# Kernel tuning notes

Measured on AMD Instinct MI355X. Metric: run time of the kernel, lower is better.

Reference implementation:

```python
import jax, jax.numpy as jnp
import numpy as np

B, DZ, DE, M, H = 4096, 2048, 128, 32, 1024
GATE_TEMP = 1.0


def setup_inputs() -> dict:
    key = jax.random.key(0)
    ks = jax.random.split(key, 6)
    s = lambda k, shape, sc: jax.random.normal(k, shape, dtype=jnp.float32) * sc
    return dict(
        z=s(ks[0], (B, DZ), 1.0),
        base_W=s(ks[1], (3, DZ), 0.02),
        base_b=jnp.zeros((3,), jnp.float32),
        gate_W=s(ks[2], (DE, DZ), 0.02),
        gate_b=jnp.zeros((DE,), jnp.float32),
        E=s(ks[3], (M, DE), 0.02),              # material embedding table
        W1=s(ks[4], (M, H, DZ + DE), 0.02),     # stacked first-layer weights
        b1=jnp.zeros((M, H), jnp.float32),
        W2=s(ks[5], (M, 3, H), 0.02),           # stacked second-layer weights
        b2=jnp.zeros((M, 3), jnp.float32),
    )


def _l2norm(x, eps=1e-12):
    # matches F.normalize(dim=-1): x / max(||x||_2, eps)
    n = jnp.linalg.norm(x, axis=-1, keepdims=True)
    return x / jnp.maximum(n, eps)


def reference(z, base_W, base_b, gate_W, gate_b, E, W1, b1, W2, b2):
    dz = z.shape[1]
    # base head: [B, 3]
    b = z @ base_W.T + base_b
    # gate similarities (routing logits): [B, M]
    q = _l2norm(z @ gate_W.T + gate_b)
    sims = q @ _l2norm(E).T
    # Per-material 2-layer MLP on cat([z, E_m]) fused as grouped GEMMs.
    # Split W1 into the z-part and embedding-part of the concat input.
    W1z, W1e = W1[:, :, :dz], W1[:, :, dz:]
    emb_term = jnp.einsum('me,mhe->mh', E, W1e)        # [M, H], shared across batch
    h = jax.nn.gelu(
        jnp.einsum('bi,mhi->bmh', z, W1z) + emb_term[None] + b1[None],
        approximate=False,
    )                                                   # [B, M, H]
    delta = jnp.einsum('bmh,moh->bmo', h, W2) + b2[None]  # [B, M, 3]
    # scale_delta_by_gate=False path; dropout inactive at inference.
    L = (b[:, None, :] + delta).reshape(z.shape[0], -1)   # [B, 3*M]
    return L, sims
```

## Files before the change

### kernel.cpp

```cpp
#include <hip/hip_runtime.h>
#include <hip/hip_bf16.h>
#include <math.h>

#define B_ROWS 4096
#define DZ     2048
#define DE     128
#define M_EXP  32
#define H_DIM  1024
#define NBIG   32768
#define NEXTRA 256
#define NTOT   (NBIG + NEXTRA)
#define W1_LD  (DZ + DE)

typedef _Float16 half8 __attribute__((ext_vector_type(8)));
typedef float    f32x4 __attribute__((ext_vector_type(4)));

#define AS1 __attribute__((address_space(1)))
#define AS3 __attribute__((address_space(3)))

__device__ __forceinline__ void async_copy16(const void* g, void* l) {
  __builtin_amdgcn_global_load_lds((const AS1 void*)g, (AS3 void*)l, 16, 0, 0);
}

__device__ __forceinline__ half8 cvt8(const float4& a, const float4& b) {
  half8 h = {(_Float16)a.x, (_Float16)a.y, (_Float16)a.z, (_Float16)a.w,
             (_Float16)b.x, (_Float16)b.y, (_Float16)b.z, (_Float16)b.w};
  return h;
}

__device__ __forceinline__ float gelu_f(float x) {
  float u = fabsf(x) * 0.70710678118654752f;
  float t = 1.0f / fmaf(0.3275911f, u, 1.0f);
  float poly = t * fmaf(t, fmaf(t, fmaf(t, fmaf(t, 1.061405429f, -1.453152027f),
                                        1.421413741f), -0.284496736f), 0.254829592f);
  float er = 1.0f - poly * __expf(-u * u);
  er = copysignf(er, x);
  return 0.5f * x * (1.0f + er);
}

__global__ __launch_bounds__(256) void k_cvt_z(const float* __restrict__ z,
                                               _Float16* __restrict__ zh) {
  long i = ((long)blockIdx.x * 256 + threadIdx.x) * 8;
  float4 a = *(const float4*)(z + i);
  float4 b = *(const float4*)(z + i + 4);
  *(half8*)(zh + i) = cvt8(a, b);
}

__global__ __launch_bounds__(256) void k_cvt_w1(const float* __restrict__ W1,
                                                const float* __restrict__ E,
                                                const float* __restrict__ b1,
                                                _Float16* __restrict__ W1h,
                                                float* __restrict__ hbias) {
  const long n = blockIdx.x;
  const int  t = threadIdx.x;
  const float* src = W1 + n * W1_LD;
  float4 a = *(const float4*)(src + t * 8);
  float4 b = *(const float4*)(src + t * 8 + 4);
  *(half8*)(W1h + n * DZ + t * 8) = cvt8(a, b);
  if (t < 32) {
    int m = (int)(n >> 10);
    float4 w = *(const float4*)(src + DZ + t * 4);
    float4 e = *(const float4*)(E + m * DE + t * 4);
    float p = w.x * e.x + w.y * e.y + w.z * e.z + w.w * e.w;
    p += __shfl_xor(p, 16);
    p += __shfl_xor(p, 8);
    p += __shfl_xor(p, 4);
    p += __shfl_xor(p, 2);
    p += __shfl_xor(p, 1);
    if (t == 0) hbias[n] = p + b1[n];
  }
}

__global__ __launch_bounds__(256) void k_cvt_small(const float* __restrict__ gate_W,
                                                   const float* __restrict__ base_W,
                                                   _Float16* __restrict__ W1h) {
  int r = blockIdx.x;
  int t = threadIdx.x;
  const float* src = nullptr;
  if (r < 128)       src = gate_W + (long)r * DZ;
  else if (r < 131)  src = base_W + (long)(r - 128) * DZ;
  _Float16* dst = W1h + (long)(NBIG + r) * DZ + t * 8;
  if (src) {
    float4 a = *(const float4*)(src + t * 8);
    float4 b = *(const float4*)(src + t * 8 + 4);
    *(half8*)dst = cvt8(a, b);
  } else {
    half8 zv = {(_Float16)0, (_Float16)0, (_Float16)0, (_Float16)0,
                (_Float16)0, (_Float16)0, (_Float16)0, (_Float16)0};
    *(half8*)dst = zv;
  }
}

__global__ __launch_bounds__(256, 2) void k_gemm(const _Float16* __restrict__ A,
                                                 const _Float16* __restrict__ Bm,
                                                 const float* __restrict__ hbias,
                                                 const float* __restrict__ W2,
                                                 float* __restrict__ Lout,
                                                 float* __restrict__ qraw) {
  __shared__ _Float16 sm[3][12288];

  int flat = blockIdx.y * gridDim.x + blockIdx.x;
  int wg   = (flat & 7) * 516 + (flat >> 3);
  const int tN = wg >> 5;
  const int tM = wg & 31;

  const int tid = threadIdx.x;
  const int w = tid >> 6, l = tid & 63;
  const int wm = w >> 1, wn = w & 1;
  const int rl = l & 15, lg = l >> 4;

  const int srow  = tid >> 2;
  const int sgoff = ((tid & 3) ^ ((srow >> 1) & 3)) * 8;
  const _Float16* gA = A  + (long)(tM * 128 + srow) * DZ + sgoff;
  const _Float16* gB = Bm + (long)(tN * 256 + srow) * DZ + sgoff;

#define STAGE_A(sb, kt) do { \
    async_copy16(gA + (kt) * 32,            &sm[sb][tid * 8]); \
    async_copy16(gA + 64 * DZ + (kt) * 32,  &sm[sb][2048 + tid * 8]); } while (0)
#define STAGE_B0(sb, kt) do { \
    async_copy16(gB + (kt) * 32,            &sm[sb][4096 + tid * 8]); \
    async_copy16(gB + 64 * DZ + (kt) * 32,  &sm[sb][6144 + tid * 8]); } while (0)
#define STAGE_B1(sb, kt) do { \
    async_copy16(gB + 128 * DZ + (kt) * 32, &sm[sb][8192 + tid * 8]); \
    async_copy16(gB + 192 * DZ + (kt) * 32, &sm[sb][10240 + tid * 8]); } while (0)

  const int aswz  = (lg ^ ((rl >> 1) & 3)) * 8;
  const int offA0 = (wm * 64 + rl) * 32 + aswz;
  const int offB0 = 4096 + (wn * 128 + rl) * 32 + aswz;

  half8 af[4], bf03[4], bf47[4];
  f32x4 acc[4][8];
  f32x4 z4 = {0.f, 0.f, 0.f, 0.f};
#pragma unroll
  for (int i = 0; i < 4; ++i)
#pragma unroll
    for (int j = 0; j < 8; ++j) acc[i][j] = z4;

#define RD_AF(sl) do { _Pragma("unroll") for (int _i = 0; _i < 4; ++_i) \
    af[_i] = *(const half8*)&sm[sl][offA0 + _i * 512]; } while (0)
#define RD_B03(sl) do { _Pragma("unroll") for (int _j = 0; _j < 4; ++_j) \
    bf03[_j] = *(const half8*)&sm[sl][offB0 + _j * 512]; } while (0)
#define RD_B47(sl) do { _Pragma("unroll") for (int _j = 0; _j < 4; ++_j) \
    bf47[_j] = *(const half8*)&sm[sl][offB0 + (4 + _j) * 512]; } while (0)

#define MFMA_J03() do { __builtin_amdgcn_s_setprio(1); \
    _Pragma("unroll") for (int _i = 0; _i < 4; ++_i) \
    _Pragma("unroll") for (int _j = 0; _j < 4; ++_j) \
      acc[_i][_j] = __builtin_amdgcn_mfma_f32_16x16x32_f16(af[_i], bf03[_j], acc[_i][_j], 0, 0, 0); \
    __builtin_amdgcn_s_setprio(0); } while (0)
#define MFMA_J47() do { __builtin_amdgcn_s_setprio(1); \
    _Pragma("unroll") for (int _i = 0; _i < 4; ++_i) \
    _Pragma("unroll") for (int _j = 0; _j < 4; ++_j) \
      acc[_i][4 + _j] = __builtin_amdgcn_mfma_f32_16x16x32_f16(af[_i], bf47[_j], acc[_i][4 + _j], 0, 0, 0); \
    __builtin_amdgcn_s_setprio(0); } while (0)

#define BAR() do { asm volatile("" ::: "memory"); __builtin_amdgcn_s_barrier(); asm volatile("" ::: "memory"); } while (0)
#define VM6 asm volatile("s_waitcnt vmcnt(6)" ::: "memory")
#define VM0 asm volatile("s_waitcnt vmcnt(0)" ::: "memory")

#define TILE_FULL(sl, s2, kt2) do { \
    BAR(); \
    RD_AF(sl); RD_B03(sl); RD_B47(sl); \
    STAGE_A(s2, kt2); STAGE_B0(s2, kt2); STAGE_B1(s2, kt2); \
    VM6; \
    MFMA_J03(); MFMA_J47(); } while (0)
#define TILE_NOST(sl, CERT) do { \
    BAR(); \
    RD_AF(sl); RD_B03(sl); RD_B47(sl); \
    CERT; \
    MFMA_J03(); MFMA_J47(); } while (0)

  STAGE_A(0, 0); STAGE_B0(0, 0); STAGE_B1(0, 0);
  STAGE_A(1, 1); STAGE_B0(1, 1); STAGE_B1(1, 1);
  VM6;

#pragma unroll 1
  for (int n = 0; n < 20; ++n) {
    const int t3 = 3 * n;
    TILE_FULL(0, 2, t3 + 2);
    TILE_FULL(1, 0, t3 + 3);
    TILE_FULL(2, 1, t3 + 4);
  }
  TILE_FULL(0, 2, 62);
  TILE_FULL(1, 0, 63);
  TILE_NOST(2, VM0);
  TILE_NOST(0, );

  if (tN < 128) {
    const int m = tN >> 2;
    float hb[8], w2v[3][8];
#pragma unroll
    for (int j = 0; j < 8; ++j) {
      int gcol = tN * 256 + wn * 128 + j * 16 + rl;
      int he   = gcol & (H_DIM - 1);
      hb[j] = hbias[gcol];
#pragma unroll
      for (int o = 0; o < 3; ++o) w2v[o][j] = W2[((long)m * 3 + o) * H_DIM + he];
    }
#pragma unroll
    for (int i = 0; i < 4; ++i) {
      const int growb = tM * 128 + wm * 64 + i * 16 + lg * 4;
#pragma unroll
      for (int r = 0; r < 4; ++r) {
        int grow = growb + r;
        float hv[8];
#pragma unroll
        for (int j = 0; j < 8; ++j) hv[j] = gelu_f(acc[i][j][r] + hb[j]);
#pragma unroll
        for (int o = 0; o < 3; ++o) {
          float p = 0.f;
#pragma unroll
          for (int j = 0; j < 8; ++j) p = fmaf(hv[j], w2v[o][j], p);
          p += __shfl_xor(p, 1);
          p += __shfl_xor(p, 2);
          p += __shfl_xor(p, 4);
          p += __shfl_xor(p, 8);
          if (rl == o) atomicAdd(&Lout[(long)grow * 96 + m * 3 + o], p);
        }
      }
    }
  } else {
#pragma unroll
    for (int i = 0; i < 4; ++i) {
      const int growb = tM * 128 + wm * 64 + i * 16 + lg * 4;
#pragma unroll
      for (int r = 0; r < 4; ++r) {
        int grow = growb + r;
        int c0 = wn * 128 + rl;
#pragma unroll
        for (int j = 0; j < 8; ++j)
          qraw[(long)grow * 256 + c0 + j * 16] = acc[i][j][r];
      }
    }
  }
}

__global__ __launch_bounds__(128) void k_post(const float* __restrict__ qraw,
                                              const float* __restrict__ gate_b,
                                              const float* __restrict__ base_b,
                                              const float* __restrict__ E,
                                              const float* __restrict__ b2,
                                              float* __restrict__ out) {
  const int b = blockIdx.x;
  const int t = threadIdx.x;
  __shared__ float qs[DE];
  __shared__ float invE[M_EXP];
  __shared__ float wsum[2];
  __shared__ float pA[M_EXP], pB[M_EXP];

  if (t < 32) {
    float ss = 0.f;
    const float* er = E + t * DE;
    for (int e = 0; e < DE; ++e) { float v = er[e]; ss += v * v; }
    invE[t] = 1.0f / fmaxf(sqrtf(ss), 1e-12f);
  }

  float val = qraw[(long)b * 256 + t] + gate_b[t];
  float ss = val * val;
  ss += __shfl_xor(ss, 1);  ss += __shfl_xor(ss, 2);  ss += __shfl_xor(ss, 4);
  ss += __shfl_xor(ss, 8);  ss += __shfl_xor(ss, 16); ss += __shfl_xor(ss, 32);
  if ((t & 63) == 0) wsum[t >> 6] = ss;
  __syncthreads();
  float inv = 1.0f / fmaxf(sqrtf(wsum[0] + wsum[1]), 1e-12f);
  qs[t] = val * inv;
  __syncthreads();

  {
    int m = t & 31, hf = t >> 5;
    const float* er = E + m * DE + hf * 32;
    const float* qq = qs + hf * 32;
    float p = 0.f;
#pragma unroll
    for (int e = 0; e < 32; ++e) p += qq[e] * er[e];
    p += __shfl_xor(p, 32);
    if (t < 32) pA[m] = p;
    else if (t >= 64 && t < 96) pB[m] = p;
    __syncthreads();
    if (t < 32) out[(long)B_ROWS * 96 + (long)b * 32 + t] = (pA[t] + pB[t]) * invE[t];
  }

  if (t < 96) {
    int o = t % 3;
    float bv = qraw[(long)b * 256 + 128 + o] + base_b[o];
    out[(long)b * 96 + t] += bv + b2[t];
  }
}

extern "C" void kernel_launch(void* const* d_in, const int* in_sizes, int n_in,
                              void* d_out, int out_size, void* d_ws, size_t ws_size,
                              hipStream_t stream) {
  const float* z      = (const float*)d_in[0];
  const float* base_W = (const float*)d_in[1];
  const float* base_b = (const float*)d_in[2];
  const float* gate_W = (const float*)d_in[3];
  const float* gate_b = (const float*)d_in[4];
  const float* E      = (const float*)d_in[5];
  const float* W1     = (const float*)d_in[6];
  const float* b1     = (const float*)d_in[7];
  const float* W2     = (const float*)d_in[8];
  const float* b2     = (const float*)d_in[9];
  float* out = (float*)d_out;

  char* ws = (char*)d_ws;
  const size_t off_zh    = 0;
  const size_t off_w1h   = off_zh  + (size_t)B_ROWS * DZ * 2;
  const size_t off_hbias = off_w1h + (size_t)NTOT * DZ * 2;
  const size_t off_qraw  = off_hbias + (size_t)NBIG * 4;
  _Float16* zh    = (_Float16*)(ws + off_zh);
  _Float16* W1h   = (_Float16*)(ws + off_w1h);
  float*    hbias = (float*)(ws + off_hbias);
  float*    qraw  = (float*)(ws + off_qraw);

  hipMemsetAsync(d_out, 0, (size_t)B_ROWS * 96 * sizeof(float), stream);

  k_cvt_z<<<(B_ROWS * DZ) / (256 * 8), 256, 0, stream>>>(z, zh);
  k_cvt_w1<<<NBIG, 256, 0, stream>>>(W1, E, b1, W1h, hbias);
  k_cvt_small<<<NEXTRA, 256, 0, stream>>>(gate_W, base_W, W1h);
  k_gemm<<<dim3(129, 32), 256, 0, stream>>>(zh, W1h, hbias, W2, out, qraw);
  k_post<<<B_ROWS, 128, 0, stream>>>(qraw, gate_b, base_b, E, b2, out);
}
```

Before: 780.9 us.

## Split GEMM tile across 8 waves with smaller per-wave 64x64 subtiles

Raises the GEMM workgroup from 256 to 512 threads (8 waves in a 2x4 layout), so each wave computes a 64x64 output subtile instead of 64x128. Each thread now issues three async LDS copies per stage instead of six, the accumulator count halves, and the launch bound targets more resident waves to hide latency. It also drops the s_setprio hints around the MFMA bursts. The cost is more LDS fragment reads per MFMA (A fragments are read by twice as many waves) and more barrier participants. Occupancy is still limited by the 72KB of shared memory per block.

```diff
diff --git a/kernel.cpp b/kernel.cpp
--- a/kernel.cpp
+++ b/kernel.cpp
@@ -91,7 +91,7 @@
   }
 }
 
-__global__ __launch_bounds__(256, 2) void k_gemm(const _Float16* __restrict__ A,
+__global__ __launch_bounds__(512, 4) void k_gemm(const _Float16* __restrict__ A,
                                                  const _Float16* __restrict__ Bm,
                                                  const float* __restrict__ hbias,
                                                  const float* __restrict__ W2,
@@ -106,7 +106,7 @@
 
   const int tid = threadIdx.x;
   const int w = tid >> 6, l = tid & 63;
-  const int wm = w >> 1, wn = w & 1;
+  const int wm = w >> 2, wn = w & 3;
   const int rl = l & 15, lg = l >> 4;
 
   const int srow  = tid >> 2;
@@ -114,65 +114,54 @@
   const _Float16* gA = A  + (long)(tM * 128 + srow) * DZ + sgoff;
   const _Float16* gB = Bm + (long)(tN * 256 + srow) * DZ + sgoff;
 
-#define STAGE_A(sb, kt) do { \
+#define STAGE(sb, kt) do { \
     async_copy16(gA + (kt) * 32,            &sm[sb][tid * 8]); \
-    async_copy16(gA + 64 * DZ + (kt) * 32,  &sm[sb][2048 + tid * 8]); } while (0)
-#define STAGE_B0(sb, kt) do { \
     async_copy16(gB + (kt) * 32,            &sm[sb][4096 + tid * 8]); \
-    async_copy16(gB + 64 * DZ + (kt) * 32,  &sm[sb][6144 + tid * 8]); } while (0)
-#define STAGE_B1(sb, kt) do { \
-    async_copy16(gB + 128 * DZ + (kt) * 32, &sm[sb][8192 + tid * 8]); \
-    async_copy16(gB + 192 * DZ + (kt) * 32, &sm[sb][10240 + tid * 8]); } while (0)
+    async_copy16(gB + 128 * DZ + (kt) * 32, &sm[sb][8192 + tid * 8]); } while (0)
 
   const int aswz  = (lg ^ ((rl >> 1) & 3)) * 8;
   const int offA0 = (wm * 64 + rl) * 32 + aswz;
-  const int offB0 = 4096 + (wn * 128 + rl) * 32 + aswz;
-
-  half8 af[4], bf03[4], bf47[4];
-  f32x4 acc[4][8];
+  const int offB0 = 4096 + (wn * 64 + rl) * 32 + aswz;
+
+  half8 af[4], bf[4];
+  f32x4 acc[4][4];
   f32x4 z4 = {0.f, 0.f, 0.f, 0.f};
 #pragma unroll
   for (int i = 0; i < 4; ++i)
 #pragma unroll
-    for (int j = 0; j < 8; ++j) acc[i][j] = z4;
-
-#define RD_AF(sl) do { _Pragma("unroll") for (int _i = 0; _i < 4; ++_i) \
-    af[_i] = *(const half8*)&sm[sl][offA0 + _i * 512]; } while (0)
-#define RD_B03(sl) do { _Pragma("unroll") for (int _j = 0; _j < 4; ++_j) \
-    bf03[_j] = *(const half8*)&sm[sl][offB0 + _j * 512]; } while (0)
-#define RD_B47(sl) do { _Pragma("unroll") for (int _j = 0; _j < 4; ++_j) \
-    bf47[_j] = *(const half8*)&sm[sl][offB0 + (4 + _j) * 512]; } while (0)
-
-#define MFMA_J03() do { __builtin_amdgcn_s_setprio(1); \
+    for (int j = 0; j < 4; ++j) acc[i][j] = z4;
+
+#define RD_FR(sl) do { \
+    _Pragma("unroll") for (int _i = 0; _i < 4; ++_i) \
+      af[_i] = *(const half8*)&sm[sl][offA0 + _i * 512]; \
+    _Pragma("unroll") for (int _j = 0; _j < 4; ++_j) \
+      bf[_j] = *(const half8*)&sm[sl][offB0 + _j * 512]; } while (0)
+
+#define MFMA16() do { \
     _Pragma("unroll") for (int _i = 0; _i < 4; ++_i) \
     _Pragma("unroll") for (int _j = 0; _j < 4; ++_j) \
-      acc[_i][_j] = __builtin_amdgcn_mfma_f32_16x16x32_f16(af[_i], bf03[_j], acc[_i][_j], 0, 0, 0); \
-    __builtin_amdgcn_s_setprio(0); } while (0)
-#define MFMA_J47() do { __builtin_amdgcn_s_setprio(1); \
-    _Pragma("unroll") for (int _i = 0; _i < 4; ++_i) \
-    _Pragma("unroll") for (int _j = 0; _j < 4; ++_j) \
-      acc[_i][4 + _j] = __builtin_amdgcn_mfma_f32_16x16x32_f16(af[_i], bf47[_j], acc[_i][4 + _j], 0, 0, 0); \
-    __builtin_amdgcn_s_setprio(0); } while (0)
+      acc[_i][_j] = __builtin_amdgcn_mfma_f32_16x16x32_f16(af[_i], bf[_j], acc[_i][_j], 0, 0, 0); \
+  } while (0)
 
 #define BAR() do { asm volatile("" ::: "memory"); __builtin_amdgcn_s_barrier(); asm volatile("" ::: "memory"); } while (0)
-#define VM6 asm volatile("s_waitcnt vmcnt(6)" ::: "memory")
+#define VM3 asm volatile("s_waitcnt vmcnt(3)" ::: "memory")
 #define VM0 asm volatile("s_waitcnt vmcnt(0)" ::: "memory")
 
 #define TILE_FULL(sl, s2, kt2) do { \
     BAR(); \
-    RD_AF(sl); RD_B03(sl); RD_B47(sl); \
-    STAGE_A(s2, kt2); STAGE_B0(s2, kt2); STAGE_B1(s2, kt2); \
-    VM6; \
-    MFMA_J03(); MFMA_J47(); } while (0)
+    RD_FR(sl); \
+    STAGE(s2, kt2); \
+    VM3; \
+    MFMA16(); } while (0)
 #define TILE_NOST(sl, CERT) do { \
     BAR(); \
-    RD_AF(sl); RD_B03(sl); RD_B47(sl); \
+    RD_FR(sl); \
     CERT; \
-    MFMA_J03(); MFMA_J47(); } while (0)
-
-  STAGE_A(0, 0); STAGE_B0(0, 0); STAGE_B1(0, 0);
-  STAGE_A(1, 1); STAGE_B0(1, 1); STAGE_B1(1, 1);
-  VM6;
+    MFMA16(); } while (0)
+
+  STAGE(0, 0);
+  STAGE(1, 1);
+  VM3;
 
 #pragma unroll 1
   for (int n = 0; n < 20; ++n) {
@@ -188,10 +177,10 @@
 
   if (tN < 128) {
     const int m = tN >> 2;
-    float hb[8], w2v[3][8];
-#pragma unroll
-    for (int j = 0; j < 8; ++j) {
-      int gcol = tN * 256 + wn * 128 + j * 16 + rl;
+    float hb[4], w2v[3][4];
+#pragma unroll
+    for (int j = 0; j < 4; ++j) {
+      int gcol = tN * 256 + wn * 64 + j * 16 + rl;
       int he   = gcol & (H_DIM - 1);
       hb[j] = hbias[gcol];
 #pragma unroll
@@ -203,14 +192,12 @@
 #pragma unroll
       for (int r = 0; r < 4; ++r) {
         int grow = growb + r;
-        float hv[8];
-#pragma unroll
-        for (int j = 0; j < 8; ++j) hv[j] = gelu_f(acc[i][j][r] + hb[j]);
+        float hv[4];
+#pragma unroll
+        for (int j = 0; j < 4; ++j) hv[j] = gelu_f(acc[i][j][r] + hb[j]);
 #pragma unroll
         for (int o = 0; o < 3; ++o) {
-          float p = 0.f;
-#pragma unroll
-          for (int j = 0; j < 8; ++j) p = fmaf(hv[j], w2v[o][j], p);
+          float p = hv[0] * w2v[o][0] + hv[1] * w2v[o][1] + hv[2] * w2v[o][2] + hv[3] * w2v[o][3];
           p += __shfl_xor(p, 1);
           p += __shfl_xor(p, 2);
           p += __shfl_xor(p, 4);
@@ -226,9 +213,9 @@
 #pragma unroll
       for (int r = 0; r < 4; ++r) {
         int grow = growb + r;
-        int c0 = wn * 128 + rl;
-#pragma unroll
-        for (int j = 0; j < 8; ++j)
+        int c0 = wn * 64 + rl;
+#pragma unroll
+        for (int j = 0; j < 4; ++j)
           qraw[(long)grow * 256 + c0 + j * 16] = acc[i][j][r];
       }
     }
@@ -316,6 +303,6 @@
   k_cvt_z<<<(B_ROWS * DZ) / (256 * 8), 256, 0, stream>>>(z, zh);
   k_cvt_w1<<<NBIG, 256, 0, stream>>>(W1, E, b1, W1h, hbias);
   k_cvt_small<<<NEXTRA, 256, 0, stream>>>(gate_W, base_W, W1h);
-  k_gemm<<<dim3(129, 32), 256, 0, stream>>>(zh, W1h, hbias, W2, out, qraw);
+  k_gemm<<<dim3(129, 32), 512, 0, stream>>>(zh, W1h, hbias, W2, out, qraw);
   k_post<<<B_ROWS, 128, 0, stream>>>(qraw, gate_b, base_b, E, b2, out);
 }
```

Measured after the change: 821.7 us. 1.05x slower.
